# Kernel optimization log

Measured on AMD Instinct MI355X. Metric: run time of the kernel, lower is better.

Reference implementation:

```python
import jax, jax.numpy as jnp
import numpy as np

DIM = 768
HEADS = 12
HEAD_DIM = DIM // HEADS
HIDDEN = int(DIM * 4.0)
EPS = 1e-5


def _layernorm(x, g, b):
    mu = jnp.mean(x, axis=-1, keepdims=True)
    var = jnp.mean(jnp.square(x - mu), axis=-1, keepdims=True)
    return (x - mu) * jax.lax.rsqrt(var + EPS) * g + b


def setup_inputs() -> dict:
    key = jax.random.key(0)
    ks = jax.random.split(key, 8)
    s_in = 1.0 / np.sqrt(DIM)
    s_hid = 1.0 / np.sqrt(HIDDEN)
    return {
        "x": jax.random.normal(ks[0], (2, 2048, DIM), dtype=jnp.float32),
        "ln1_g": jnp.ones((DIM,), jnp.float32),
        "ln1_b": jnp.zeros((DIM,), jnp.float32),
        "w_qkv": jax.random.normal(ks[1], (DIM, 3 * DIM), jnp.float32) * s_in,
        "w_proj": jax.random.normal(ks[2], (DIM, DIM), jnp.float32) * s_in,
        "b_proj": jnp.zeros((DIM,), jnp.float32),
        "ln2_g": jnp.ones((DIM,), jnp.float32),
        "ln2_b": jnp.zeros((DIM,), jnp.float32),
        "w_fc1": jax.random.normal(ks[3], (DIM, HIDDEN), jnp.float32) * s_in,
        "b_fc1": jnp.zeros((HIDDEN,), jnp.float32),
        "w_fc2": jax.random.normal(ks[4], (HIDDEN, DIM), jnp.float32) * s_hid,
        "b_fc2": jnp.zeros((DIM,), jnp.float32),
    }


def reference(x, ln1_g, ln1_b, w_qkv, w_proj, b_proj, ln2_g, ln2_b, w_fc1, b_fc1, w_fc2, b_fc2):
    b, n, c = x.shape
    scale = HEAD_DIM ** -0.5

    # --- attention branch ---
    h = _layernorm(x, ln1_g, ln1_b)
    qkv = (h @ w_qkv).reshape(b, n, 3, HEADS, HEAD_DIM)
    q, k, v = jnp.moveaxis(qkv, 2, 0)          # each [b, n, H, hd]
    attn = jnp.einsum("bqhd,bkhd->bhqk", q, k) * scale
    attn = jax.nn.softmax(attn, axis=-1)       # [b, H, n, n] (naive, materialized)
    o = jnp.einsum("bhqk,bkhd->bqhd", attn, v).reshape(b, n, c)
    x = x + o @ w_proj + b_proj

    # --- MLP branch ---
    h2 = _layernorm(x, ln2_g, ln2_b)
    m = jax.nn.gelu(h2 @ w_fc1 + b_fc1, approximate=False)
    x = x + m @ w_fc2 + b_fc2
    return x
```

## Files before the change

### kernel.cpp

```cpp
#include <hip/hip_runtime.h>
#include <math.h>


typedef unsigned short u16;
typedef __attribute__((ext_vector_type(8))) short short8;
typedef __attribute__((ext_vector_type(4))) float f32x4;

#define TOKENS 4096
#define DIM    768
#define QKV_N  2304
#define HID    3072
#define NSEQ   2048
#define NHEAD  12
#define HDIM   64

__device__ __forceinline__ float bf2f(u16 u) {
  union { unsigned i; float f; } v; v.i = ((unsigned)u) << 16; return v.f;
}
__device__ __forceinline__ u16 f2bf(float f) {
  union { float f; unsigned i; } v; v.f = f;
  unsigned r = v.i + 0x7fffu + ((v.i >> 16) & 1u);
  return (u16)(r >> 16);
}
__device__ __forceinline__ u16 f2bf_trunc(float f) {
  union { float f; unsigned i; } v; v.f = f;
  return (u16)(v.i >> 16);
}

__device__ __forceinline__ void async_copy16(const u16* g, u16* l) {
  __builtin_amdgcn_global_load_lds(
      (const __attribute__((address_space(1))) unsigned int*)(unsigned long long)g,
      (__attribute__((address_space(3))) unsigned int*)(unsigned int)(unsigned long long)l,
      16, 0, 0);
}

__global__ __launch_bounds__(256) void prep_kernel(
    const float* __restrict__ x, const float* __restrict__ g,
    const float* __restrict__ b, u16* __restrict__ h,
    const float* __restrict__ in0, u16* __restrict__ out0,
    const float* __restrict__ in1, u16* __restrict__ out1,
    const float* __restrict__ in2, u16* __restrict__ out2,
    const float* __restrict__ in3, u16* __restrict__ out3) {
  const int tid = threadIdx.x;
  if (blockIdx.x < 1024) {
    int wave = tid >> 6, lane = tid & 63;
    int token = blockIdx.x * 4 + wave;
    float v[12];
    const float4* xr = (const float4*)(x + (size_t)token * DIM);
#pragma unroll
    for (int w = 0; w < 3; w++) {
      float4 q = xr[lane + w * 64];
      v[w * 4 + 0] = q.x; v[w * 4 + 1] = q.y; v[w * 4 + 2] = q.z; v[w * 4 + 3] = q.w;
    }
    float s = 0.f;
#pragma unroll
    for (int i = 0; i < 12; i++) s += v[i];
#pragma unroll
    for (int off = 32; off > 0; off >>= 1) s += __shfl_xor(s, off);
    float mu = s * (1.0f / DIM);
    float ss = 0.f;
#pragma unroll
    for (int i = 0; i < 12; i++) { float d = v[i] - mu; ss += d * d; }
#pragma unroll
    for (int off = 32; off > 0; off >>= 1) ss += __shfl_xor(ss, off);
    float rs = rsqrtf(ss * (1.0f / DIM) + 1e-5f);
    ushort4* orow = (ushort4*)(h + (size_t)token * DIM);
    const float4* g4 = (const float4*)g;
    const float4* b4 = (const float4*)b;
#pragma unroll
    for (int w = 0; w < 3; w++) {
      float4 gq = g4[lane + w * 64], bq = b4[lane + w * 64];
      ushort4 o;
      o.x = f2bf((v[w * 4 + 0] - mu) * rs * gq.x + bq.x);
      o.y = f2bf((v[w * 4 + 1] - mu) * rs * gq.y + bq.y);
      o.z = f2bf((v[w * 4 + 2] - mu) * rs * gq.z + bq.z);
      o.w = f2bf((v[w * 4 + 3] - mu) * rs * gq.w + bq.w);
      orow[lane + w * 64] = o;
    }
    return;
  }
  __shared__ u16 t[32][33];
  int bid = blockIdx.x - 1024, rem;
  const float* in; u16* out; int R, C;
  if (bid < 1728)      { in = in0; out = out0; R = 768;  C = 2304; rem = bid; }
  else if (bid < 2304) { in = in1; out = out1; R = 768;  C = 768;  rem = bid - 1728; }
  else if (bid < 4608) { in = in2; out = out2; R = 768;  C = 3072; rem = bid - 2304; }
  else                 { in = in3; out = out3; R = 3072; C = 768;  rem = bid - 4608; }
  int c0 = (rem % (C / 32)) * 32, r0 = (rem / (C / 32)) * 32;
  int tx = tid & 31, ty = tid >> 5;
#pragma unroll
  for (int i = 0; i < 4; i++)
    t[ty + i * 8][tx] = f2bf(in[(size_t)(r0 + ty + i * 8) * C + c0 + tx]);
  __syncthreads();
#pragma unroll
  for (int i = 0; i < 4; i++)
    out[(size_t)(c0 + ty + i * 8) * R + r0 + tx] = t[tx][ty + i * 8];
}

__global__ __launch_bounds__(256) void ln_kernel(const u16* __restrict__ xin,
                                                 const float* __restrict__ g,
                                                 const float* __restrict__ b,
                                                 u16* __restrict__ out) {
  int wave = threadIdx.x >> 6, lane = threadIdx.x & 63;
  int token = blockIdx.x * 4 + wave;
  float v[12];
  const ushort4* xr = (const ushort4*)(xin + (size_t)token * DIM);
#pragma unroll
  for (int w = 0; w < 3; w++) {
    ushort4 q = xr[lane + w * 64];
    v[w * 4 + 0] = bf2f(q.x); v[w * 4 + 1] = bf2f(q.y);
    v[w * 4 + 2] = bf2f(q.z); v[w * 4 + 3] = bf2f(q.w);
  }
  float s = 0.f;
#pragma unroll
  for (int i = 0; i < 12; i++) s += v[i];
#pragma unroll
  for (int off = 32; off > 0; off >>= 1) s += __shfl_xor(s, off);
  float mu = s * (1.0f / DIM);
  float ss = 0.f;
#pragma unroll
  for (int i = 0; i < 12; i++) { float d = v[i] - mu; ss += d * d; }
#pragma unroll
  for (int off = 32; off > 0; off >>= 1) ss += __shfl_xor(ss, off);
  float rs = rsqrtf(ss * (1.0f / DIM) + 1e-5f);

  ushort4* orow = (ushort4*)(out + (size_t)token * DIM);
  const float4* g4 = (const float4*)g;
  const float4* b4 = (const float4*)b;
#pragma unroll
  for (int w = 0; w < 3; w++) {
    float4 gq = g4[lane + w * 64], bq = b4[lane + w * 64];
    ushort4 o;
    o.x = f2bf((v[w * 4 + 0] - mu) * rs * gq.x + bq.x);
    o.y = f2bf((v[w * 4 + 1] - mu) * rs * gq.y + bq.y);
    o.z = f2bf((v[w * 4 + 2] - mu) * rs * gq.z + bq.z);
    o.w = f2bf((v[w * 4 + 3] - mu) * rs * gq.w + bq.w);
    orow[lane + w * 64] = o;
  }
}

template <int BM, int BN, int EPI>
__global__ __launch_bounds__(256, 3) void gemm_bt(
    const u16* __restrict__ A, const u16* __restrict__ BT,
    void* __restrict__ Cout, const float* __restrict__ bias,
    const void* __restrict__ resid, int M, int N, int K,
    u16* __restrict__ vtb) {
  constexpr int MT = BM / 32, NT = BN / 32;
  constexpr int ACH = BM / 16;
  constexpr int CPW = (BM + BN) / 64;
  __shared__ __align__(16) u16 Alds[2][BM * 32];
  __shared__ __align__(16) u16 Blds[2][BN * 32];
  const int tid = threadIdx.x;
  const int lane = tid & 63, wave = tid >> 6;
  const int wr = wave >> 1, wc = wave & 1;
  const int bm = blockIdx.y * BM, bn = blockIdx.x * BN;
  const int c16 = lane & 15, quad = lane >> 4;
  const int l4 = lane >> 2, lc = (lane & 3) * 8;

  f32x4 acc[MT][NT];
#pragma unroll
  for (int i = 0; i < MT; i++)
#pragma unroll
    for (int j = 0; j < NT; j++) acc[i][j] = (f32x4){0.f, 0.f, 0.f, 0.f};

  const u16* gsrc[CPW];
  u16* ldst[2][CPW];
#pragma unroll
  for (int c = 0; c < CPW; c++) {
    int chunk = wave * CPW + c;
    if (chunk < ACH) {
      gsrc[c] = A + (size_t)(bm + chunk * 16 + l4) * K + lc;
      ldst[0][c] = Alds[0] + chunk * 512;
      ldst[1][c] = Alds[1] + chunk * 512;
    } else {
      int bc = chunk - ACH;
      gsrc[c] = BT + (size_t)(bn + bc * 16 + l4) * K + lc;
      ldst[0][c] = Blds[0] + bc * 512;
      ldst[1][c] = Blds[1] + bc * 512;
    }
  }

#pragma unroll
  for (int c = 0; c < CPW; c++) async_copy16(gsrc[c], ldst[0][c]);

  const int nit = K / 32;
  for (int it = 0; it < nit; it++) {
    const int cur = it & 1;
    __syncthreads();
    if (it + 1 < nit) {
      const int kk = (it + 1) * 32;
#pragma unroll
      for (int c = 0; c < CPW; c++) async_copy16(gsrc[c] + kk, ldst[cur ^ 1][c]);
    }
    short8 af[MT], bfr[NT];
#pragma unroll
    for (int mt = 0; mt < MT; mt++)
      af[mt] = *(const short8*)(Alds[cur] + (wr * (BM / 2) + mt * 16 + c16) * 32 + quad * 8);
#pragma unroll
    for (int nt = 0; nt < NT; nt++)
      bfr[nt] = *(const short8*)(Blds[cur] + (wc * (BN / 2) + nt * 16 + c16) * 32 + quad * 8);
#pragma unroll
    for (int mt = 0; mt < MT; mt++)
#pragma unroll
      for (int nt = 0; nt < NT; nt++)
        acc[mt][nt] = __builtin_amdgcn_mfma_f32_16x16x32_bf16(af[mt], bfr[nt],
                                                              acc[mt][nt], 0, 0, 0);
  }

#pragma unroll
  for (int mt = 0; mt < MT; mt++) {
#pragma unroll
    for (int nt = 0; nt < NT; nt++) {
      int col = bn + wc * (BN / 2) + nt * 16 + c16;
      float bv = (EPI != 0) ? bias[col] : 0.f;
      int row0 = bm + wr * (BM / 2) + mt * 16 + quad * 4;
      if (EPI == 0 && col >= 2 * DIM) {
        int b = row0 >> 11;
        ushort4 pk;
        pk.x = f2bf(acc[mt][nt][0]); pk.y = f2bf(acc[mt][nt][1]);
        pk.z = f2bf(acc[mt][nt][2]); pk.w = f2bf(acc[mt][nt][3]);
        *(ushort4*)(vtb + ((size_t)b * DIM + col - 2 * DIM) * NSEQ + (row0 & 2047)) = pk;
        continue;
      }
#pragma unroll
      for (int r = 0; r < 4; r++) {
        int row = row0 + r;
        float vv = acc[mt][nt][r];
        if (EPI == 1) {
          vv += bv + ((const float*)resid)[(size_t)row * N + col];
          ((u16*)Cout)[(size_t)row * N + col] = f2bf(vv);
        } else if (EPI == 2) {
          vv += bv;
          vv = 0.5f * vv * (1.0f + erff(vv * 0.70710678118654752f));
          ((u16*)Cout)[(size_t)row * N + col] = f2bf(vv);
        } else if (EPI == 3) {
          vv += bv + bf2f(((const u16*)resid)[(size_t)row * N + col]);
          ((float*)Cout)[(size_t)row * N + col] = vv;
        } else {
          ((u16*)Cout)[(size_t)row * N + col] = f2bf(vv);
        }
      }
    }
  }
}

__global__ __launch_bounds__(256) void attn_kernel(const u16* __restrict__ qkv,
                                                   const u16* __restrict__ vt,
                                                   u16* __restrict__ o) {
  const int tid = threadIdx.x;
  const int lane = tid & 63, wave = tid >> 6;
  const int c16 = lane & 15, quad = lane >> 4;
  const int qt = blockIdx.x & 31;
  const int bh = blockIdx.x >> 5;
  const int bb = bh / NHEAD, h = bh % NHEAD;
  __shared__ __align__(16) u16 Klds[2][64 * 64];
  __shared__ __align__(16) u16 Vtlds[2][64 * 64];
  __shared__ __align__(16) u16 Plds[4][16 * 64];
  const size_t base = (size_t)bb * NSEQ * QKV_N;
  const int q0 = qt * 64 + wave * 16;

  const u16* qp = qkv + base + (size_t)(q0 + c16) * QKV_N + h * HDIM;
  short8 qf0 = *(const short8*)(qp + quad * 8);
  short8 qf1 = *(const short8*)(qp + 32 + quad * 8);

  float Ls[4] = {0.f, 0.f, 0.f, 0.f};
  f32x4 Of[4];
#pragma unroll
  for (int dt = 0; dt < 4; dt++) Of[dt] = (f32x4){0.f, 0.f, 0.f, 0.f};

  const int srow = lane >> 3;
  const int schunk = (lane & 7) ^ srow;
  const int r0 = wave * 16;
  const u16* ksrc = qkv + base + (size_t)(r0 + srow) * QKV_N + DIM + h * HDIM + schunk * 8;
  const u16* vsrc = vt + ((size_t)bh * HDIM + r0 + srow) * NSEQ + schunk * 8;

  const int cswz0 = (quad ^ (c16 & 7)) * 8;
  const int cswz1 = ((quad + 4) ^ (c16 & 7)) * 8;
  const float SC = 0.18033688011112042f;

#pragma unroll
  for (int j = 0; j < 2; j++) {
    async_copy16(ksrc + (size_t)(8 * j) * QKV_N, Klds[0] + r0 * 64 + 8 * j * 64);
    async_copy16(vsrc + (size_t)(8 * j) * NSEQ, Vtlds[0] + r0 * 64 + 8 * j * 64);
  }

  for (int it = 0; it < NSEQ / 64; it++) {
    const int cur = it & 1;
    __syncthreads();
    if (it + 1 < NSEQ / 64) {
      const int kt1 = (it + 1) * 64;
      u16* kd = Klds[cur ^ 1] + r0 * 64;
      u16* vd = Vtlds[cur ^ 1] + r0 * 64;
#pragma unroll
      for (int j = 0; j < 2; j++) {
        async_copy16(ksrc + (size_t)(kt1 + 8 * j) * QKV_N, kd + 8 * j * 64);
        async_copy16(vsrc + (size_t)(8 * j) * NSEQ + kt1, vd + 8 * j * 64);
      }
    }

    f32x4 S[4];
#pragma unroll
    for (int nt = 0; nt < 4; nt++) {
      S[nt] = (f32x4){0.f, 0.f, 0.f, 0.f};
      const u16* krow = Klds[cur] + (nt * 16 + c16) * 64;
      short8 ka = *(const short8*)(krow + cswz0);
      short8 kb = *(const short8*)(krow + cswz1);
      S[nt] = __builtin_amdgcn_mfma_f32_16x16x32_bf16(qf0, ka, S[nt], 0, 0, 0);
      S[nt] = __builtin_amdgcn_mfma_f32_16x16x32_bf16(qf1, kb, S[nt], 0, 0, 0);
    }

    u16* pl = Plds[wave];
    const int el = c16 & 7, ch = c16 >> 3;
#pragma unroll
    for (int r = 0; r < 4; r++) {
      float p0 = __builtin_amdgcn_exp2f(S[0][r] * SC);
      float p1 = __builtin_amdgcn_exp2f(S[1][r] * SC);
      float p2 = __builtin_amdgcn_exp2f(S[2][r] * SC);
      float p3 = __builtin_amdgcn_exp2f(S[3][r] * SC);
      Ls[r] += (p0 + p1) + (p2 + p3);
      u16* pr = pl + (quad * 4 + r) * 64;
      const int r7 = (quad * 4 + r) & 7;
      pr[((0 + ch) ^ r7) * 8 + el] = f2bf_trunc(p0);
      pr[((2 + ch) ^ r7) * 8 + el] = f2bf_trunc(p1);
      pr[((4 + ch) ^ r7) * 8 + el] = f2bf_trunc(p2);
      pr[((6 + ch) ^ r7) * 8 + el] = f2bf_trunc(p3);
    }

    short8 pf0 = *(const short8*)(pl + c16 * 64 + cswz0);
    short8 pf1 = *(const short8*)(pl + c16 * 64 + cswz1);
#pragma unroll
    for (int dt = 0; dt < 4; dt++) {
      const u16* vrow = Vtlds[cur] + (dt * 16 + c16) * 64;
      short8 va = *(const short8*)(vrow + cswz0);
      short8 vb = *(const short8*)(vrow + cswz1);
      Of[dt] = __builtin_amdgcn_mfma_f32_16x16x32_bf16(pf0, va, Of[dt], 0, 0, 0);
      Of[dt] = __builtin_amdgcn_mfma_f32_16x16x32_bf16(pf1, vb, Of[dt], 0, 0, 0);
    }
  }

#pragma unroll
  for (int r = 0; r < 4; r++) {
    float t = Ls[r];
    t += __shfl_xor(t, 1); t += __shfl_xor(t, 2);
    t += __shfl_xor(t, 4); t += __shfl_xor(t, 8);
    Ls[r] = t;
  }

#pragma unroll
  for (int dt = 0; dt < 4; dt++)
#pragma unroll
    for (int r = 0; r < 4; r++) {
      int token = q0 + quad * 4 + r;
      float val = Of[dt][r] / Ls[r];
      o[(size_t)(bb * NSEQ + token) * DIM + h * HDIM + dt * 16 + c16] = f2bf(val);
    }
}

extern "C" void kernel_launch(void* const* d_in, const int* in_sizes, int n_in,
                              void* d_out, int out_size, void* d_ws, size_t ws_size,
                              hipStream_t stream) {
  (void)in_sizes; (void)n_in; (void)out_size; (void)ws_size;
  const float* x      = (const float*)d_in[0];
  const float* ln1_g  = (const float*)d_in[1];
  const float* ln1_b  = (const float*)d_in[2];
  const float* w_qkv  = (const float*)d_in[3];
  const float* w_proj = (const float*)d_in[4];
  const float* b_proj = (const float*)d_in[5];
  const float* ln2_g  = (const float*)d_in[6];
  const float* ln2_b  = (const float*)d_in[7];
  const float* w_fc1  = (const float*)d_in[8];
  const float* b_fc1  = (const float*)d_in[9];
  const float* w_fc2  = (const float*)d_in[10];
  const float* b_fc2  = (const float*)d_in[11];
  float* out = (float*)d_out;

  char* p = (char*)d_ws;
  u16* h_bf   = (u16*)p; p += (size_t)TOKENS * DIM * 2;
  u16* qkv_bf = (u16*)p; p += (size_t)TOKENS * QKV_N * 2;
  u16* o_bf   = (u16*)p; p += (size_t)TOKENS * DIM * 2;
  u16* x1_bf  = (u16*)p; p += (size_t)TOKENS * DIM * 2;
  u16* wprojT = (u16*)p; p += (size_t)DIM * DIM * 2;
  u16* wfc1T  = (u16*)p; p += (size_t)HID * DIM * 2;
  u16* wfc2T  = (u16*)p; p += (size_t)DIM * HID * 2;
  u16* wqkvT  = (u16*)p; p += (size_t)QKV_N * DIM * 2;
  u16* vtb    = (u16*)p; p += (size_t)TOKENS * DIM * 2;
  u16* m_bf   = qkv_bf;

  prep_kernel<<<dim3(1024 + 6912), 256, 0, stream>>>(
      x, ln1_g, ln1_b, h_bf,
      w_qkv, wqkvT, w_proj, wprojT, w_fc1, wfc1T, w_fc2, wfc2T);

  gemm_bt<64, 128, 0><<<dim3(QKV_N / 128, TOKENS / 64), 256, 0, stream>>>(
      h_bf, wqkvT, qkv_bf, nullptr, nullptr, TOKENS, QKV_N, DIM, vtb);
  attn_kernel<<<dim3(2 * NHEAD * (NSEQ / 64)), 256, 0, stream>>>(qkv_bf, vtb, o_bf);
  gemm_bt<64, 128, 1><<<dim3(DIM / 128, TOKENS / 64), 256, 0, stream>>>(
      o_bf, wprojT, x1_bf, b_proj, x, TOKENS, DIM, DIM, nullptr);
  ln_kernel<<<TOKENS / 4, 256, 0, stream>>>(x1_bf, ln2_g, ln2_b, h_bf);
  gemm_bt<128, 128, 2><<<dim3(HID / 128, TOKENS / 128), 256, 0, stream>>>(
      h_bf, wfc1T, m_bf, b_fc1, nullptr, TOKENS, HID, DIM, nullptr);
  gemm_bt<64, 128, 3><<<dim3(DIM / 128, TOKENS / 64), 256, 0, stream>>>(
      m_bf, wfc2T, out, b_fc2, x1_bf, TOKENS, DIM, HID, nullptr);
}
```

Before: 283.6 us.

## Reorder block mapping for weight reuse and load K=64 per barrier step

Launches GEMMs on a 1D grid with M-index fastest so neighbouring blocks share the same weight tile in L2, and reorders attention blocks so heads vary fastest. The GEMM main loop drops the prefetch-next-tile double buffering and instead loads two K=32 slices into both LDS buffers, synchronises, then computes both. This halves loop iterations but gives up overlap of global loads with MFMA work, relying on multiple resident blocks to hide latency.

```diff
diff --git a/kernel.cpp b/kernel.cpp
--- a/kernel.cpp
+++ b/kernel.cpp
@@ -153,7 +153,9 @@
   const int tid = threadIdx.x;
   const int lane = tid & 63, wave = tid >> 6;
   const int wr = wave >> 1, wc = wave & 1;
-  const int bm = blockIdx.y * BM, bn = blockIdx.x * BN;
+  const int nby = M / BM;
+  const int by = blockIdx.x % nby, bx = blockIdx.x / nby;
+  const int bm = by * BM, bn = bx * BN;
   const int c16 = lane & 15, quad = lane >> 4;
   const int l4 = lane >> 2, lc = (lane & 3) * 8;
 
@@ -164,47 +166,47 @@
     for (int j = 0; j < NT; j++) acc[i][j] = (f32x4){0.f, 0.f, 0.f, 0.f};
 
   const u16* gsrc[CPW];
-  u16* ldst[2][CPW];
+  u16* ldst[CPW];
+  int hstep[CPW];
 #pragma unroll
   for (int c = 0; c < CPW; c++) {
     int chunk = wave * CPW + c;
     if (chunk < ACH) {
       gsrc[c] = A + (size_t)(bm + chunk * 16 + l4) * K + lc;
-      ldst[0][c] = Alds[0] + chunk * 512;
-      ldst[1][c] = Alds[1] + chunk * 512;
+      ldst[c] = Alds[0] + chunk * 512;
+      hstep[c] = BM * 32;
     } else {
       int bc = chunk - ACH;
       gsrc[c] = BT + (size_t)(bn + bc * 16 + l4) * K + lc;
-      ldst[0][c] = Blds[0] + bc * 512;
-      ldst[1][c] = Blds[1] + bc * 512;
-    }
-  }
-
-#pragma unroll
-  for (int c = 0; c < CPW; c++) async_copy16(gsrc[c], ldst[0][c]);
-
-  const int nit = K / 32;
-  for (int it = 0; it < nit; it++) {
-    const int cur = it & 1;
+      ldst[c] = Blds[0] + bc * 512;
+      hstep[c] = BN * 32;
+    }
+  }
+
+  for (int kk = 0; kk < K; kk += 64) {
     __syncthreads();
-    if (it + 1 < nit) {
-      const int kk = (it + 1) * 32;
-#pragma unroll
-      for (int c = 0; c < CPW; c++) async_copy16(gsrc[c] + kk, ldst[cur ^ 1][c]);
-    }
-    short8 af[MT], bfr[NT];
-#pragma unroll
-    for (int mt = 0; mt < MT; mt++)
-      af[mt] = *(const short8*)(Alds[cur] + (wr * (BM / 2) + mt * 16 + c16) * 32 + quad * 8);
-#pragma unroll
-    for (int nt = 0; nt < NT; nt++)
-      bfr[nt] = *(const short8*)(Blds[cur] + (wc * (BN / 2) + nt * 16 + c16) * 32 + quad * 8);
-#pragma unroll
-    for (int mt = 0; mt < MT; mt++)
+#pragma unroll
+    for (int c = 0; c < CPW; c++) {
+      async_copy16(gsrc[c] + kk, ldst[c]);
+      async_copy16(gsrc[c] + kk + 32, ldst[c] + hstep[c]);
+    }
+    __syncthreads();
+#pragma unroll
+    for (int ks = 0; ks < 2; ks++) {
+      short8 af[MT], bfr[NT];
+#pragma unroll
+      for (int mt = 0; mt < MT; mt++)
+        af[mt] = *(const short8*)(Alds[ks] + (wr * (BM / 2) + mt * 16 + c16) * 32 + quad * 8);
 #pragma unroll
       for (int nt = 0; nt < NT; nt++)
-        acc[mt][nt] = __builtin_amdgcn_mfma_f32_16x16x32_bf16(af[mt], bfr[nt],
-                                                              acc[mt][nt], 0, 0, 0);
+        bfr[nt] = *(const short8*)(Blds[ks] + (wc * (BN / 2) + nt * 16 + c16) * 32 + quad * 8);
+#pragma unroll
+      for (int mt = 0; mt < MT; mt++)
+#pragma unroll
+        for (int nt = 0; nt < NT; nt++)
+          acc[mt][nt] = __builtin_amdgcn_mfma_f32_16x16x32_bf16(af[mt], bfr[nt],
+                                                                acc[mt][nt], 0, 0, 0);
+    }
   }
 
 #pragma unroll
@@ -250,8 +252,8 @@
   const int tid = threadIdx.x;
   const int lane = tid & 63, wave = tid >> 6;
   const int c16 = lane & 15, quad = lane >> 4;
-  const int qt = blockIdx.x & 31;
-  const int bh = blockIdx.x >> 5;
+  const int bh = blockIdx.x % (2 * NHEAD);
+  const int qt = blockIdx.x / (2 * NHEAD);
   const int bb = bh / NHEAD, h = bh % NHEAD;
   __shared__ __align__(16) u16 Klds[2][64 * 64];
   __shared__ __align__(16) u16 Vtlds[2][64 * 64];
@@ -390,14 +392,14 @@
       x, ln1_g, ln1_b, h_bf,
       w_qkv, wqkvT, w_proj, wprojT, w_fc1, wfc1T, w_fc2, wfc2T);
 
-  gemm_bt<64, 128, 0><<<dim3(QKV_N / 128, TOKENS / 64), 256, 0, stream>>>(
+  gemm_bt<64, 128, 0><<<dim3((QKV_N / 128) * (TOKENS / 64)), 256, 0, stream>>>(
       h_bf, wqkvT, qkv_bf, nullptr, nullptr, TOKENS, QKV_N, DIM, vtb);
   attn_kernel<<<dim3(2 * NHEAD * (NSEQ / 64)), 256, 0, stream>>>(qkv_bf, vtb, o_bf);
-  gemm_bt<64, 128, 1><<<dim3(DIM / 128, TOKENS / 64), 256, 0, stream>>>(
+  gemm_bt<64, 128, 1><<<dim3((DIM / 128) * (TOKENS / 64)), 256, 0, stream>>>(
       o_bf, wprojT, x1_bf, b_proj, x, TOKENS, DIM, DIM, nullptr);
   ln_kernel<<<TOKENS / 4, 256, 0, stream>>>(x1_bf, ln2_g, ln2_b, h_bf);
-  gemm_bt<128, 128, 2><<<dim3(HID / 128, TOKENS / 128), 256, 0, stream>>>(
+  gemm_bt<128, 128, 2><<<dim3((HID / 128) * (TOKENS / 128)), 256, 0, stream>>>(
       h_bf, wfc1T, m_bf, b_fc1, nullptr, TOKENS, HID, DIM, nullptr);
-  gemm_bt<64, 128, 3><<<dim3(DIM / 128, TOKENS / 64), 256, 0, stream>>>(
+  gemm_bt<64, 128, 3><<<dim3((DIM / 128) * (TOKENS / 64)), 256, 0, stream>>>(
       m_bf, wfc2T, out, b_fc2, x1_bf, TOKENS, DIM, HID, nullptr);
 }
```

Measured after the change: 270.2 us. -4.7%, faster.
